# Performance work log

Measured on AMD Instinct MI355X. Metric: run time of the kernel, lower is better.

Reference implementation:

```python
import jax, jax.numpy as jnp
import numpy as np

NUM_HEADS = 4
GROUPS = 8
EPS = 1e-5


def setup_inputs() -> dict:
    key = jax.random.key(0)
    ks = jax.random.split(key, 8)
    B, C, H, W = 8, 512, 64, 64
    L, E = 77, 768
    std = 0.02
    return {
        "x": jax.random.normal(ks[0], (B, C, H, W), jnp.float32),
        "text_emb": jax.random.normal(ks[1], (B, L, E), jnp.float32),
        "attention_mask": jax.random.randint(ks[2], (B, L), 0, 2, jnp.int32),
        "Wq_w": jax.random.normal(ks[3], (C, C), jnp.float32) * std,
        "Wq_b": jnp.zeros((C,), jnp.float32),
        "Wk_w": jax.random.normal(ks[4], (C, E), jnp.float32) * std,
        "Wk_b": jnp.zeros((C,), jnp.float32),
        "Wv_w": jax.random.normal(ks[5], (C, E), jnp.float32) * std,
        "Wv_b": jnp.zeros((C,), jnp.float32),
        "gn_scale": jnp.ones((C,), jnp.float32),
        "gn_bias": jnp.zeros((C,), jnp.float32),
    }


def reference(x, text_emb, attention_mask, Wq_w, Wq_b, Wk_w, Wk_b, Wv_w, Wv_b, gn_scale, gn_bias):
    B, C, H, W = x.shape
    dh = C // NUM_HEADS
    scale = dh ** -0.5

    # [B, HW, C] queries from image features
    x_flat = x.reshape(B, C, H * W).transpose(0, 2, 1)
    Q = x_flat @ Wq_w.T + Wq_b                 # [B, S, C]
    K = text_emb @ Wk_w.T + Wk_b               # [B, L, C]
    V = text_emb @ Wv_w.T + Wv_b               # [B, L, C]

    def split_heads(t):
        Bt, T, _ = t.shape
        return t.reshape(Bt, T, NUM_HEADS, dh).transpose(0, 2, 1, 3)  # [B, h, T, dh]

    Qh, Kh, Vh = split_heads(Q), split_heads(K), split_heads(V)

    scores = jnp.einsum("bhqd,bhkd->bhqk", Qh, Kh) * scale  # [B, h, S, L]
    mask = (attention_mask == 0)[:, None, None, :]
    scores = jnp.where(mask, -jnp.inf, scores)
    probs = jax.nn.softmax(scores, axis=-1)
    # dropout layers are identity in eval mode
    attn = jnp.einsum("bhqk,bhkd->bhqd", probs, Vh)          # [B, h, S, dh]

    out = attn.transpose(0, 2, 1, 3).reshape(B, H * W, C)    # [B, S, C]
    out = out.transpose(0, 2, 1).reshape(B, C, H, W)

    # GroupNorm(8 groups, affine) over (C/G, H, W) per group
    g = out.reshape(B, GROUPS, -1)
    mean = g.mean(axis=-1, keepdims=True)
    var = g.var(axis=-1, keepdims=True)
    g = (g - mean) * jax.lax.rsqrt(var + EPS)
    out = g.reshape(B, C, H, W) * gn_scale[None, :, None, None] + gn_bias[None, :, None, None]
    return out
```

## Files before the change

### kernel.cpp

```cpp
#include <hip/hip_runtime.h>
#include <hip/hip_bf16.h>
#include <cstdint>


typedef __attribute__((ext_vector_type(8))) short short8;
typedef __attribute__((ext_vector_type(4))) short short4v;
typedef __attribute__((ext_vector_type(4))) float f32x4;

#define DEV __device__ __forceinline__

DEV float bf2f(unsigned short u){ union{uint32_t i; float f;} x; x.i = ((uint32_t)u) << 16; return x.f; }
DEV unsigned short f2bf(float f){ __hip_bfloat16 h = __float2bfloat16(f); return *reinterpret_cast<unsigned short*>(&h); }
DEV short8 ld8(const unsigned short* p){ return *reinterpret_cast<const short8*>(p); }
DEV f32x4 ldf4(const float* p){ return *reinterpret_cast<const f32x4*>(p); }

#if defined(__has_builtin)
#if __has_builtin(__builtin_amdgcn_global_load_lds)
#define HAVE_ASYNC_LDS 1
#endif
#endif

__global__ __launch_bounds__(256) void k_fat(const float* __restrict__ x,
                                             unsigned short* __restrict__ xT,
                                             const float* __restrict__ text,
                                             const float* __restrict__ Wk,
                                             const float* __restrict__ Wkb,
                                             const float* __restrict__ Wv,
                                             const float* __restrict__ Wvb,
                                             unsigned short* __restrict__ wsK,
                                             unsigned short* __restrict__ wsVt,
                                             const float* __restrict__ Wq,
                                             unsigned short* __restrict__ wsWqT,
                                             int b0, int s_base, int slen, int SB){
  __shared__ unsigned short U[10368];
  const int tid = threadIdx.x;
  const int bx = blockIdx.x, by = blockIdx.y, bz = blockIdx.z;
  const int bg = b0 + bz;

  if (bx < 64){
    if (bx * 64 >= slen) return;
    unsigned short* t = U;
    const int s0 = s_base + bx * 64, c0 = by * 64;
    #pragma unroll
    for (int it = 0; it < 2; ++it){
      int slot = tid + it * 256;
      int r = slot >> 3, sg = slot & 7;
      int sw = sg ^ (r >> 3);
      const float* src = &x[((size_t)(bg * 512 + c0 + r)) * 4096 + s0 + sg * 8];
      f32x4 a = ldf4(src), b = ldf4(src + 4);
      short8 v;
      #pragma unroll
      for (int j = 0; j < 4; ++j){ v[j] = (short)f2bf(a[j]); v[j + 4] = (short)f2bf(b[j]); }
      *reinterpret_cast<short8*>(&t[r * 72 + sw * 8]) = v;
    }
    __syncthreads();
    #pragma unroll
    for (int it = 0; it < 2; ++it){
      int slot = tid + it * 256;
      int j = slot >> 3, i8 = slot & 7;
      short8 v;
      #pragma unroll
      for (int q = 0; q < 8; ++q){
        int c = i8 * 8 + q;
        int sw = (j >> 3) ^ i8;
        v[q] = (short)t[c * 72 + sw * 8 + (j & 7)];
      }
      *reinterpret_cast<short8*>(&xT[((size_t)(bz * slen) + bx * 64 + j) * 512 + c0 + i8 * 8]) = v;
    }
  } else if (bx < 66){
    unsigned short* At = U;
    unsigned short* Bt = U + 5760;
    const int wave = tid >> 6, lane = tid & 63;
    const int m16 = lane & 15, quad = lane >> 4;
    const int uc = (bx - 64) * 8 + by;
    const int u0 = uc * 64;
    const bool isK = (u0 < 512);
    const float* W  = isK ? Wk  : Wv;
    const float* Wb = isK ? Wkb : Wvb;
    const int c0 = u0 & 511;
    const int c  = c0 + wave * 16 + m16;
    f32x4 acc[5];
    #pragma unroll
    for (int mt = 0; mt < 5; ++mt) acc[mt] = (f32x4){0.f, 0.f, 0.f, 0.f};
    for (int kc = 0; kc < 12; ++kc){
      const int e0 = kc * 64;
      #pragma unroll
      for (int it = 0; it < 9; ++it){
        int slot = tid + it * 256;
        if (slot < 1280){
          int row = slot >> 4, e4 = (slot & 15) * 4;
          f32x4 v = (row < 77) ? ldf4(&text[((size_t)(bg * 77 + row)) * 768 + e0 + e4])
                               : (f32x4){0.f, 0.f, 0.f, 0.f};
          short4v o;
          #pragma unroll
          for (int j = 0; j < 4; ++j) o[j] = (short)f2bf(v[j]);
          *reinterpret_cast<short4v*>(&At[row * 72 + e4]) = o;
        } else {
          int bs = slot - 1280;
          int row = bs >> 4, e4 = (bs & 15) * 4;
          f32x4 v = ldf4(&W[((size_t)(c0 + row)) * 768 + e0 + e4]);
          short4v o;
          #pragma unroll
          for (int j = 0; j < 4; ++j) o[j] = (short)f2bf(v[j]);
          *reinterpret_cast<short4v*>(&Bt[row * 72 + e4]) = o;
        }
      }
      __syncthreads();
      #pragma unroll
      for (int kk = 0; kk < 64; kk += 32){
        short8 bf_ = *reinterpret_cast<const short8*>(&Bt[(wave * 16 + m16) * 72 + kk + quad * 8]);
        #pragma unroll
        for (int mt = 0; mt < 5; ++mt){
          short8 af_ = *reinterpret_cast<const short8*>(&At[(mt * 16 + m16) * 72 + kk + quad * 8]);
          acc[mt] = __builtin_amdgcn_mfma_f32_16x16x32_bf16(af_, bf_, acc[mt], 0, 0, 0);
        }
      }
      __syncthreads();
    }
    const float bias = Wb[c];
    if (isK){
      #pragma unroll
      for (int mt = 0; mt < 5; ++mt)
        #pragma unroll
        for (int r = 0; r < 4; ++r){
          int l = mt * 16 + quad * 4 + r;
          if (l < 77) wsK[((size_t)(bz * 77 + l)) * 512 + c] = f2bf(acc[mt][r] + bias);
        }
    } else {
      unsigned short* vr = &wsVt[((size_t)(bz * 512 + c)) * 96];
      #pragma unroll
      for (int mt = 0; mt < 5; ++mt){
        short4v pk;
        #pragma unroll
        for (int r = 0; r < 4; ++r) pk[r] = (short)f2bf(acc[mt][r] + bias);
        *reinterpret_cast<short4v*>(&vr[mt * 16 + quad * 4]) = pk;
      }
      short4v z = {};
      *reinterpret_cast<short4v*>(&vr[80 + quad * 4]) = z;
    }
  } else {
    unsigned short* t = U;
    const int nb = 8 * SB;
    const int p  = by + bz * 8;
    for (int tile = p; tile < 64; tile += nb){
      const int ti = tile >> 3, tj = tile & 7;
      #pragma unroll
      for (int it = 0; it < 2; ++it){
        int slot = tid + it * 256;
        int r = slot >> 3, sg = slot & 7;
        int sw = sg ^ (r >> 3);
        const float* src = &Wq[((size_t)(tj * 64 + r)) * 512 + ti * 64 + sg * 8];
        f32x4 a = ldf4(src), b2 = ldf4(src + 4);
        short8 v;
        #pragma unroll
        for (int j = 0; j < 4; ++j){ v[j] = (short)f2bf(a[j]); v[j + 4] = (short)f2bf(b2[j]); }
        *reinterpret_cast<short8*>(&t[r * 72 + sw * 8]) = v;
      }
      __syncthreads();
      #pragma unroll
      for (int it = 0; it < 2; ++it){
        int slot = tid + it * 256;
        int j = slot >> 3, i8 = slot & 7;
        short8 v;
        #pragma unroll
        for (int q = 0; q < 8; ++q){
          int dd = i8 * 8 + q;
          int sw = (j >> 3) ^ i8;
          v[q] = (short)t[dd * 72 + sw * 8 + (j & 7)];
        }
        *reinterpret_cast<short8*>(&wsWqT[((size_t)(ti * 64 + j)) * 512 + tj * 64 + i8 * 8]) = v;
      }
      __syncthreads();
    }
  }
}

__global__ __launch_bounds__(256) void k1b(const unsigned short* __restrict__ wsWqT,
                                           const unsigned short* __restrict__ wsK,
                                           const float* __restrict__ Wqb,
                                           unsigned short* __restrict__ wsKWq,
                                           float* __restrict__ kbias){
  const int tid = threadIdx.x;
  const int wave = tid >> 6, lane = tid & 63;
  const int m16 = lane & 15, quad = lane >> 4;
  const int cq = blockIdx.x, h = blockIdx.y, bz = blockIdx.z;
  const int cbase = cq * 128 + wave * 32;

  f32x4 acc[2][5];
  #pragma unroll
  for (int mt = 0; mt < 2; ++mt)
    #pragma unroll
    for (int nt = 0; nt < 5; ++nt) acc[mt][nt] = (f32x4){0.f, 0.f, 0.f, 0.f};

  #pragma unroll
  for (int ks = 0; ks < 4; ++ks){
    short8 aw[2];
    #pragma unroll
    for (int mt = 0; mt < 2; ++mt)
      aw[mt] = ld8(&wsWqT[(size_t)(cbase + mt * 16 + m16) * 512 + h * 128 + ks * 32 + quad * 8]);
    #pragma unroll
    for (int nt = 0; nt < 5; ++nt){
      int l = nt * 16 + m16;
      short8 bk = {};
      if (l < 77) bk = ld8(&wsK[((size_t)(bz * 77 + l)) * 512 + h * 128 + ks * 32 + quad * 8]);
      #pragma unroll
      for (int mt = 0; mt < 2; ++mt)
        acc[mt][nt] = __builtin_amdgcn_mfma_f32_16x16x32_bf16(aw[mt], bk, acc[mt][nt], 0, 0, 0);
    }
  }
  #pragma unroll
  for (int mt = 0; mt < 2; ++mt)
    #pragma unroll
    for (int nt = 0; nt < 5; ++nt){
      int l = nt * 16 + m16;
      short4v pk;
      #pragma unroll
      for (int r = 0; r < 4; ++r) pk[r] = (short)f2bf(acc[mt][nt][r]);
      *reinterpret_cast<short4v*>(&wsKWq[((size_t)((bz * 4 + h) * 80 + l)) * 512 + cbase + mt * 16 + quad * 4]) = pk;
    }
  if (cq == 0 && tid < 80){
    int l = tid;
    float kb = 0.f;
    if (l < 77){
      #pragma unroll
      for (int d = 0; d < 128; d += 8){
        short8 kv = ld8(&wsK[((size_t)(bz * 77 + l)) * 512 + h * 128 + d]);
        f32x4 wa = ldf4(&Wqb[h * 128 + d]);
        f32x4 wb = ldf4(&Wqb[h * 128 + d + 4]);
        #pragma unroll
        for (int j = 0; j < 4; ++j){
          kb += bf2f((unsigned short)kv[j]) * wa[j];
          kb += bf2f((unsigned short)kv[j + 4]) * wb[j];
        }
      }
    }
    kbias[(bz * 4 + h) * 80 + l] = kb;
  }
}

__global__ __launch_bounds__(256, 3) void k2_attn(const unsigned short* __restrict__ xT,
                                                  const unsigned short* __restrict__ wsKWq,
                                                  const unsigned short* __restrict__ wsVt,
                                                  const int* __restrict__ amask,
                                                  const float* __restrict__ kbias,
                                                  float* __restrict__ out,
                                                  float* __restrict__ gnacc,
                                                  int b0, int s_base, int slen){
  __shared__ unsigned short arena[26624];
  __shared__ float maskf[96];
  unsigned short* Pt = arena;

  const int tid = threadIdx.x;
  const int wave = tid >> 6, lane = tid & 63;
  const int m16 = lane & 15, quad = lane >> 4;
  const int st = blockIdx.x, h = blockIdx.y, bz = blockIdx.z;
  const int bg = b0 + bz;
  const int s_glob = s_base + st * 128;
  const int R0 = (wave >> 1) * 64, C0 = (wave & 1) * 64;
  const int sw0 = wave * 32;
  const float scale = 0.08838834764831845f;

  if (tid < 96){
    int l = tid;
    float mbv = -30000.f;
    if (l < 77 && amask[bg * 77 + l] != 0) mbv = kbias[(bz * 4 + h) * 80 + l] * scale;
    maskf[l] = mbv;
  }

  const unsigned short* Abase = wsKWq + (size_t)((bz * 4 + h) * 80) * 512;
  const unsigned short* Bbase = xT + ((size_t)bz * slen + st * 128) * 512;

  f32x4 acc2[5][2];
  #pragma unroll
  for (int mt = 0; mt < 5; ++mt){ acc2[mt][0] = (f32x4){0.f,0.f,0.f,0.f}; acc2[mt][1] = (f32x4){0.f,0.f,0.f,0.f}; }

  auto stage = [&](int kc, int buf){
    const int sbase = buf * 13312;
    #pragma unroll
    for (int it = 0; it < 7; ++it){
      const int ubase = it * 256 + wave * 64;
      if (ubase < 1664){
        const int u = ubase + lane;
        const unsigned short* src;
        if (u < 640){
          int l = u >> 3, pos = (u & 7) ^ (l & 7);
          src = Abase + (size_t)l * 512 + kc * 64 + pos * 8;
        } else {
          int v = u - 640;
          int s = v >> 3, pos = (v & 7) ^ (s & 7);
          src = Bbase + (size_t)s * 512 + kc * 64 + pos * 8;
        }
#ifdef HAVE_ASYNC_LDS
        __builtin_amdgcn_global_load_lds((const __attribute__((address_space(1))) void*)src,
                                         (__attribute__((address_space(3))) void*)&arena[sbase + ubase * 8],
                                         16, 0, 0);
#else
        *reinterpret_cast<short8*>(&arena[sbase + (ubase + lane) * 8]) = ld8(src);
#endif
      }
    }
  };

  auto compute = [&](int buf){
    const int ab = buf * 13312;
    const int bb = ab + 5120;
    #pragma unroll
    for (int kk = 0; kk < 2; ++kk){
      short8 af[5], bfr[2];
      #pragma unroll
      for (int mt = 0; mt < 5; ++mt){
        int l = mt * 16 + m16;
        int p = (kk * 4 + quad) ^ (l & 7);
        af[mt] = *reinterpret_cast<const short8*>(&arena[ab + l * 64 + p * 8]);
      }
      #pragma unroll
      for (int nt = 0; nt < 2; ++nt){
        int s = sw0 + nt * 16 + m16;
        int p = (kk * 4 + quad) ^ (s & 7);
        bfr[nt] = *reinterpret_cast<const short8*>(&arena[bb + s * 64 + p * 8]);
      }
      #pragma unroll
      for (int mt = 0; mt < 5; ++mt)
        #pragma unroll
        for (int nt = 0; nt < 2; ++nt)
          acc2[mt][nt] = __builtin_amdgcn_mfma_f32_16x16x32_bf16(af[mt], bfr[nt], acc2[mt][nt], 0, 0, 0);
    }
  };

  stage(0, 0);
  __syncthreads();
  #pragma unroll
  for (int kc = 0; kc < 8; ++kc){
    if (kc < 7) stage(kc + 1, (kc + 1) & 1);
    compute(kc & 1);
    __syncthreads();
  }

  {
    float mb[5][4];
    #pragma unroll
    for (int mt = 0; mt < 5; ++mt)
      #pragma unroll
      for (int r = 0; r < 4; ++r) mb[mt][r] = maskf[mt * 16 + quad * 4 + r];
    #pragma unroll
    for (int nt = 0; nt < 2; ++nt){
      float sv[5][4]; float mx = -3e38f;
      #pragma unroll
      for (int mt = 0; mt < 5; ++mt)
        #pragma unroll
        for (int r = 0; r < 4; ++r){
          float v = acc2[mt][nt][r] * scale + mb[mt][r];
          sv[mt][r] = v; mx = fmaxf(mx, v);
        }
      mx = fmaxf(mx, __shfl_xor(mx, 16)); mx = fmaxf(mx, __shfl_xor(mx, 32));
      float sum = 0.f;
      #pragma unroll
      for (int mt = 0; mt < 5; ++mt)
        #pragma unroll
        for (int r = 0; r < 4; ++r){ float e = __expf(sv[mt][r] - mx); sv[mt][r] = e; sum += e; }
      sum += __shfl_xor(sum, 16); sum += __shfl_xor(sum, 32);
      float inv = 1.0f / sum;
      int sl = sw0 + nt * 16 + m16;
      #pragma unroll
      for (int mt = 0; mt < 5; ++mt){
        short4v pk;
        #pragma unroll
        for (int r = 0; r < 4; ++r) pk[r] = (short)f2bf(sv[mt][r] * inv);
        *reinterpret_cast<short4v*>(&Pt[sl * 104 + mt * 16 + quad * 4]) = pk;
      }
      short4v z = {};
      *reinterpret_cast<short4v*>(&Pt[sl * 104 + 80 + quad * 4]) = z;
    }
  }
  __syncthreads();

  f32x4 acc3[4][4];
  #pragma unroll
  for (int mt = 0; mt < 4; ++mt)
    #pragma unroll
    for (int nt = 0; nt < 4; ++nt) acc3[mt][nt] = (f32x4){0.f, 0.f, 0.f, 0.f};
  const unsigned short* Vb = wsVt + (size_t)(bz * 512 + h * 128) * 96;
  #pragma unroll
  for (int ks = 0; ks < 3; ++ks){
    short8 av[4], bp[4];
    #pragma unroll
    for (int mt = 0; mt < 4; ++mt)
      av[mt] = ld8(&Vb[(size_t)(R0 + mt * 16 + m16) * 96 + ks * 32 + quad * 8]);
    #pragma unroll
    for (int nt = 0; nt < 4; ++nt)
      bp[nt] = *reinterpret_cast<const short8*>(&Pt[(C0 + nt * 16 + m16) * 104 + ks * 32 + quad * 8]);
    #pragma unroll
    for (int mt = 0; mt < 4; ++mt)
      #pragma unroll
      for (int nt = 0; nt < 4; ++nt)
        acc3[mt][nt] = __builtin_amdgcn_mfma_f32_16x16x32_bf16(av[mt], bp[nt], acc3[mt][nt], 0, 0, 0);
  }
  float sum = 0.f, ssq = 0.f;
  #pragma unroll
  for (int mt = 0; mt < 4; ++mt)
    #pragma unroll
    for (int nt = 0; nt < 4; ++nt){
      int sidx = s_glob + C0 + nt * 16 + m16;
      #pragma unroll
      for (int r = 0; r < 4; ++r){
        float v = acc3[mt][nt][r];
        sum += v; ssq += v * v;
        int d = h * 128 + R0 + mt * 16 + quad * 4 + r;
        out[(size_t)(bg * 512 + d) * 4096 + sidx] = v;
      }
    }
  #pragma unroll
  for (int off = 1; off < 64; off <<= 1){ sum += __shfl_xor(sum, off); ssq += __shfl_xor(ssq, off); }
  if (lane == 0){
    int g = h * 2 + (R0 >> 6);
    atomicAdd(&gnacc[(bg * 8 + g) * 2],     sum);
    atomicAdd(&gnacc[(bg * 8 + g) * 2 + 1], ssq);
  }
}

__global__ __launch_bounds__(256) void k3_gn(float* __restrict__ out,
                                             const float* __restrict__ gnacc,
                                             const float* __restrict__ gns,
                                             const float* __restrict__ gnb){
  const int bx = blockIdx.x;
  const int b = bx >> 9, c = bx & 511;
  const int g = c >> 6;
  const float s  = gnacc[(b * 8 + g) * 2];
  const float ss = gnacc[(b * 8 + g) * 2 + 1];
  const float invN = 1.f / 262144.f;
  const float mean = s * invN;
  const float var  = ss * invN - mean * mean;
  const float rstd = rsqrtf(fmaxf(var, 0.f) + 1e-5f);
  const float a  = rstd * gns[c];
  const float bb = gnb[c] - mean * a;
  const size_t base = (size_t)bx * 4096;
  #pragma unroll
  for (int p = 0; p < 4; ++p){
    size_t off = base + p * 1024 + threadIdx.x * 4;
    f32x4 v = ldf4(&out[off]);
    f32x4 o;
    #pragma unroll
    for (int j = 0; j < 4; ++j) o[j] = v[j] * a + bb;
    *reinterpret_cast<f32x4*>(&out[off]) = o;
  }
}

extern "C" void kernel_launch(void* const* d_in, const int* in_sizes, int n_in,
                              void* d_out, int out_size, void* d_ws, size_t ws_size,
                              hipStream_t stream){
  (void)in_sizes; (void)n_in; (void)out_size;
  const float* x    = (const float*)d_in[0];
  const float* text = (const float*)d_in[1];
  const int*   am   = (const int*)d_in[2];
  const float* Wq   = (const float*)d_in[3];
  const float* Wqb  = (const float*)d_in[4];
  const float* Wk   = (const float*)d_in[5];
  const float* Wkb  = (const float*)d_in[6];
  const float* Wv   = (const float*)d_in[7];
  const float* Wvb  = (const float*)d_in[8];
  const float* gns  = (const float*)d_in[9];
  const float* gnb  = (const float*)d_in[10];
  float* out = (float*)d_out;

  auto need = [](int SB, int SLEN) -> size_t {
    return 512ull + 524288ull + (size_t)SB * 506112ull + (size_t)SB * SLEN * 1024ull;
  };
  int SB = 8, SLEN = 4096;
  if      (ws_size >= need(8, 4096)) { SB = 8; SLEN = 4096; }
  else if (ws_size >= need(4, 4096)) { SB = 4; SLEN = 4096; }
  else if (ws_size >= need(2, 4096)) { SB = 2; SLEN = 4096; }
  else if (ws_size >= need(1, 4096)) { SB = 1; SLEN = 4096; }
  else if (ws_size >= need(1, 1024)) { SB = 1; SLEN = 1024; }
  else                               { SB = 1; SLEN = 256;  }

  uint8_t* ws = (uint8_t*)d_ws;
  float*          gnacc = (float*)ws;
  unsigned short* wsWqT = (unsigned short*)(ws + 512);
  unsigned short* wsK   = wsWqT + 512 * 512;
  unsigned short* wsVt  = wsK  + (size_t)SB * 77 * 512;
  unsigned short* wsKWq = wsVt + (size_t)SB * 512 * 96;
  float*          kbias = (float*)(wsKWq + (size_t)SB * 4 * 80 * 512);
  unsigned short* xT    = (unsigned short*)(kbias + (size_t)SB * 4 * 80);

  hipMemsetAsync(gnacc, 0, 128 * sizeof(float), stream);
  for (int b0 = 0; b0 < 8; b0 += SB){
    for (int s_base = 0; s_base < 4096; s_base += SLEN){
      k_fat<<<dim3(67, 8, SB), 256, 0, stream>>>(x, xT, text, Wk, Wkb, Wv, Wvb,
                                                 wsK, wsVt, Wq, wsWqT, b0, s_base, SLEN, SB);
      if (s_base == 0)
        k1b<<<dim3(4, 4, SB), 256, 0, stream>>>(wsWqT, wsK, Wqb, wsKWq, kbias);
      k2_attn<<<dim3(SLEN / 128, 4, SB), 256, 0, stream>>>(xT, wsKWq, wsVt, am, kbias,
                                                           out, gnacc, b0, s_base, SLEN);
    }
  }
  k3_gn<<<4096, 256, 0, stream>>>(out, gnacc, gns, gnb);
}
```

Measured before the change: 137.5 us.

## Load B operand directly to registers and shrink LDS to raise occupancy

The xT (B) tiles are now loaded by each wave straight from global memory into registers, double-buffered, instead of being staged through LDS. Only the shared K·Wq tile goes through LDS, which halves the arena and lets launch bounds rise from 3 to 4 blocks per SM. The first V fragment is also prefetched before the softmax so its latency overlaps. The risks are higher register pressure under the tighter bound and global B loads that are less coalesced than the old LDS staging.

```diff
diff --git a/kernel.cpp b/kernel.cpp
--- a/kernel.cpp
+++ b/kernel.cpp
@@ -238,7 +238,7 @@
   }
 }
 
-__global__ __launch_bounds__(256, 3) void k2_attn(const unsigned short* __restrict__ xT,
+__global__ __launch_bounds__(256, 4) void k2_attn(const unsigned short* __restrict__ xT,
                                                   const unsigned short* __restrict__ wsKWq,
                                                   const unsigned short* __restrict__ wsVt,
                                                   const int* __restrict__ amask,
@@ -246,7 +246,7 @@
                                                   float* __restrict__ out,
                                                   float* __restrict__ gnacc,
                                                   int b0, int s_base, int slen){
-  __shared__ unsigned short arena[26624];
+  __shared__ unsigned short arena[13312];
   __shared__ float maskf[96];
   unsigned short* Pt = arena;
 
@@ -268,45 +268,46 @@
   }
 
   const unsigned short* Abase = wsKWq + (size_t)((bz * 4 + h) * 80) * 512;
-  const unsigned short* Bbase = xT + ((size_t)bz * slen + st * 128) * 512;
+  const unsigned short* Bbase = xT + ((size_t)bz * slen + st * 128 + sw0) * 512;
 
   f32x4 acc2[5][2];
   #pragma unroll
   for (int mt = 0; mt < 5; ++mt){ acc2[mt][0] = (f32x4){0.f,0.f,0.f,0.f}; acc2[mt][1] = (f32x4){0.f,0.f,0.f,0.f}; }
 
-  auto stage = [&](int kc, int buf){
-    const int sbase = buf * 13312;
-    #pragma unroll
-    for (int it = 0; it < 7; ++it){
+  auto stageA = [&](int kc, int buf){
+    const int sbase = buf * 5120;
+    #pragma unroll
+    for (int it = 0; it < 3; ++it){
       const int ubase = it * 256 + wave * 64;
-      if (ubase < 1664){
+      if (ubase < 640){
         const int u = ubase + lane;
-        const unsigned short* src;
-        if (u < 640){
-          int l = u >> 3, pos = (u & 7) ^ (l & 7);
-          src = Abase + (size_t)l * 512 + kc * 64 + pos * 8;
-        } else {
-          int v = u - 640;
-          int s = v >> 3, pos = (v & 7) ^ (s & 7);
-          src = Bbase + (size_t)s * 512 + kc * 64 + pos * 8;
-        }
+        int l = u >> 3, pos = (u & 7) ^ (l & 7);
+        const unsigned short* src = Abase + (size_t)l * 512 + kc * 64 + pos * 8;
 #ifdef HAVE_ASYNC_LDS
         __builtin_amdgcn_global_load_lds((const __attribute__((address_space(1))) void*)src,
                                          (__attribute__((address_space(3))) void*)&arena[sbase + ubase * 8],
                                          16, 0, 0);
 #else
-        *reinterpret_cast<short8*>(&arena[sbase + (ubase + lane) * 8]) = ld8(src);
+        *reinterpret_cast<short8*>(&arena[sbase + u * 8]) = ld8(src);
 #endif
       }
     }
   };
 
+  short8 Breg[2][4];
+  auto loadB = [&](int kc, int buf){
+    #pragma unroll
+    for (int nt = 0; nt < 2; ++nt)
+      #pragma unroll
+      for (int kk = 0; kk < 2; ++kk)
+        Breg[buf][nt * 2 + kk] = ld8(&Bbase[(size_t)(nt * 16 + m16) * 512 + kc * 64 + kk * 32 + quad * 8]);
+  };
+
   auto compute = [&](int buf){
-    const int ab = buf * 13312;
-    const int bb = ab + 5120;
+    const int ab = buf * 5120;
     #pragma unroll
     for (int kk = 0; kk < 2; ++kk){
-      short8 af[5], bfr[2];
+      short8 af[5];
       #pragma unroll
       for (int mt = 0; mt < 5; ++mt){
         int l = mt * 16 + m16;
@@ -314,27 +315,28 @@
         af[mt] = *reinterpret_cast<const short8*>(&arena[ab + l * 64 + p * 8]);
       }
       #pragma unroll
-      for (int nt = 0; nt < 2; ++nt){
-        int s = sw0 + nt * 16 + m16;
-        int p = (kk * 4 + quad) ^ (s & 7);
-        bfr[nt] = *reinterpret_cast<const short8*>(&arena[bb + s * 64 + p * 8]);
-      }
-      #pragma unroll
       for (int mt = 0; mt < 5; ++mt)
         #pragma unroll
         for (int nt = 0; nt < 2; ++nt)
-          acc2[mt][nt] = __builtin_amdgcn_mfma_f32_16x16x32_bf16(af[mt], bfr[nt], acc2[mt][nt], 0, 0, 0);
+          acc2[mt][nt] = __builtin_amdgcn_mfma_f32_16x16x32_bf16(af[mt], Breg[buf][nt * 2 + kk], acc2[mt][nt], 0, 0, 0);
     }
   };
 
-  stage(0, 0);
+  stageA(0, 0);
+  loadB(0, 0);
   __syncthreads();
   #pragma unroll
   for (int kc = 0; kc < 8; ++kc){
-    if (kc < 7) stage(kc + 1, (kc + 1) & 1);
+    if (kc < 7){ stageA(kc + 1, (kc + 1) & 1); loadB(kc + 1, (kc + 1) & 1); }
     compute(kc & 1);
     __syncthreads();
   }
+
+  const unsigned short* Vb = wsVt + (size_t)(bz * 512 + h * 128) * 96;
+  short8 av0[4];
+  #pragma unroll
+  for (int mt = 0; mt < 4; ++mt)
+    av0[mt] = ld8(&Vb[(size_t)(R0 + mt * 16 + m16) * 96 + quad * 8]);
 
   {
     float mb[5][4];
@@ -379,13 +381,13 @@
   for (int mt = 0; mt < 4; ++mt)
     #pragma unroll
     for (int nt = 0; nt < 4; ++nt) acc3[mt][nt] = (f32x4){0.f, 0.f, 0.f, 0.f};
-  const unsigned short* Vb = wsVt + (size_t)(bz * 512 + h * 128) * 96;
   #pragma unroll
   for (int ks = 0; ks < 3; ++ks){
     short8 av[4], bp[4];
     #pragma unroll
     for (int mt = 0; mt < 4; ++mt)
-      av[mt] = ld8(&Vb[(size_t)(R0 + mt * 16 + m16) * 96 + ks * 32 + quad * 8]);
+      av[mt] = (ks == 0) ? av0[mt]
+                         : ld8(&Vb[(size_t)(R0 + mt * 16 + m16) * 96 + ks * 32 + quad * 8]);
     #pragma unroll
     for (int nt = 0; nt < 4; ++nt)
       bp[nt] = *reinterpret_cast<const short8*>(&Pt[(C0 + nt * 16 + m16) * 104 + ks * 32 + quad * 8]);
```

New measurement: 138.6 us. No clear change (+0.8%).
